# Kernel optimization log

Measured on AMD Instinct MI355X. Metric: run time of the kernel, lower is better.

The kernel has to match this reference:

```python
import jax, jax.numpy as jnp
import numpy as np

BATCH = 32768
DIM = 256
NUM_LATENTS = 4096
ENTROPY_WEIGHT = 0.1
VQ_BETA = 0.25
EPS = 1e-9


def _l2_normalize(v, axis=-1, eps=1e-12):
    # matches torch F.normalize(dim=-1)
    n = jnp.linalg.norm(v, axis=axis, keepdims=True)
    return v / jnp.maximum(n, eps)


def setup_inputs() -> dict:
    key = jax.random.key(0)
    kx, kc = jax.random.split(key)
    x = jax.random.normal(kx, (BATCH, DIM), dtype=jnp.float32)
    # codebook initialized uniform(-bound, bound) then row-normalized, as in __init__
    bound = (3.0 / DIM) ** 0.5
    cb = jax.random.uniform(kc, (NUM_LATENTS, DIM), dtype=jnp.float32,
                            minval=-bound, maxval=bound)
    codebook = _l2_normalize(cb)
    return {"x": x, "codebook": codebook}


def reference(x, codebook):
    # cosine-distance nearest-code lookup
    x_norm = _l2_normalize(x)                       # [B, D]
    cb_norm = _l2_normalize(codebook)               # [K, D]
    distance = -jnp.einsum('bd,kd->bk', x_norm, cb_norm)  # [B, K]
    # dropout p=0.0 -> identity
    indices = jnp.argmin(distance, axis=-1)         # [B] int
    z = codebook[indices]                           # [B, D] gather

    # straight-through estimator
    z_q = x + jax.lax.stop_gradient(z - x)

    commit_loss = jnp.mean((x - jax.lax.stop_gradient(z)) ** 2)
    q_loss = jnp.mean((z - jax.lax.stop_gradient(x)) ** 2)

    # entropy of codebook usage
    counts = jnp.bincount(indices, length=NUM_LATENTS).astype(jnp.float32)
    probs = counts / counts.sum()
    entropy = -jnp.sum(probs * jnp.log(jnp.clip(probs, EPS)))
    entropy_loss = -entropy

    vq_loss = q_loss + VQ_BETA * commit_loss + ENTROPY_WEIGHT * entropy_loss
    return (z_q, vq_loss, q_loss, commit_loss, entropy_loss, entropy, indices)
```

## Files before the change

### kernel.cpp

```cpp
#include <hip/hip_runtime.h>
#include <math.h>

#define BATCH 32768
#define DIM   256
#define NLAT  4096

typedef _Float16 f16x8 __attribute__((ext_vector_type(8)));
typedef float    f32x16 __attribute__((ext_vector_type(16)));

#define WS_CBH    0u
#define WS_CBINV  2097152u
#define WS_KEYS   2113536u
#define WS_HIST   4210688u

__device__ inline float kdec(uint key) {
  return __uint_as_float(key & 0xFFFFF000u);
}

__device__ inline void gload_lds16(const void* g, void* l) {
  __builtin_amdgcn_global_load_lds(
      (const __attribute__((address_space(1))) void*)g,
      (__attribute__((address_space(3))) void*)l, 16, 0, 0);
}

__global__ __launch_bounds__(256) void prep_kernel(
    const float* __restrict__ x, const float* __restrict__ cb,
    float* __restrict__ cbinv, uint4* __restrict__ cbhf4,
    uint4* __restrict__ xhf4, int* __restrict__ hist) {
  __shared__ __align__(16) uint4 lds[2048];
  __shared__ float linv[64];
  int bid = blockIdx.x, tid = threadIdx.x;
  if (bid < 64) {
    int w = tid >> 6, l = tid & 63;
    int t = bid;
    for (int rr = 0; rr < 16; ++rr) {
      int row = t * 64 + w * 16 + rr;
      float4 v = ((const float4*)(cb + (size_t)row * DIM))[l];
      float s = v.x * v.x + v.y * v.y + v.z * v.z + v.w * v.w;
      #pragma unroll
      for (int m = 32; m; m >>= 1) s += __shfl_xor(s, m, 64);
      if (l == 0) {
        float inv = 1.0f / fmaxf(sqrtf(s), 1e-12f);
        linv[w * 16 + rr] = inv;
        cbinv[row] = inv;
      }
    }
    __syncthreads();
    #pragma unroll
    for (int k = 0; k < 8; ++k) {
      int g = tid * 8 + k;
      int r64 = g >> 5, c = g & 31;
      const float4* cr = (const float4*)(cb + (size_t)(t * 64 + r64) * DIM);
      float inv = linv[r64];
      float4 a = cr[c * 2], b = cr[c * 2 + 1];
      union { _Float16 h[8]; uint4 u; } pk;
      pk.h[0] = (_Float16)(a.x * inv); pk.h[1] = (_Float16)(a.y * inv);
      pk.h[2] = (_Float16)(a.z * inv); pk.h[3] = (_Float16)(a.w * inv);
      pk.h[4] = (_Float16)(b.x * inv); pk.h[5] = (_Float16)(b.y * inv);
      pk.h[6] = (_Float16)(b.z * inv); pk.h[7] = (_Float16)(b.w * inv);
      int rf = r64 >> 5, row31 = r64 & 31;
      int sl = c >> 1, lhh = c & 1;
      lds[(sl * 2 + rf) * 64 + lhh * 32 + row31] = pk.u;
    }
    __syncthreads();
    uint4* outp = cbhf4 + (size_t)t * 2048;
    #pragma unroll
    for (int k = 0; k < 8; ++k)
      outp[tid * 8 + k] = lds[tid * 8 + k];
  } else if (bid < 1088) {
    int xb = bid - 64;
    const float4* xs = (const float4*)x + (size_t)xb * 2048;
    #pragma unroll
    for (int k = 0; k < 4; ++k) {
      int g = tid * 4 + k;
      float4 a = xs[g * 2];
      float4 b = xs[g * 2 + 1];
      union { _Float16 h[8]; uint4 u; } pk;
      pk.h[0] = (_Float16)a.x; pk.h[1] = (_Float16)a.y;
      pk.h[2] = (_Float16)a.z; pk.h[3] = (_Float16)a.w;
      pk.h[4] = (_Float16)b.x; pk.h[5] = (_Float16)b.y;
      pk.h[6] = (_Float16)b.z; pk.h[7] = (_Float16)b.w;
      int row31 = g >> 5, c = g & 31;
      lds[(c >> 1) * 64 + (c & 1) * 32 + row31] = pk.u;
    }
    __syncthreads();
    uint4* outp = xhf4 + (size_t)xb * 1024;
    #pragma unroll
    for (int k = 0; k < 4; ++k)
      outp[tid * 4 + k] = lds[tid * 4 + k];
  } else {
    for (int k = tid; k < NLAT; k += 256) hist[k] = 0;
  }
}

__global__ __launch_bounds__(256, 2) void vq_gemm_kernel(
    const char* __restrict__ xhf, const char* __restrict__ cbhf,
    uint* __restrict__ keys) {
  __shared__ __align__(16) char smem[65536];

  const int tid = threadIdx.x;
  const int w = tid >> 6, l = tid & 63;
  const int l31 = l & 31, lh = l >> 5;
  const int bb = blockIdx.x >> 2, q = blockIdx.x & 3;
  const int wrow0 = bb * 128 + w * 32;
  const int cbase = q * 1024;
  const uint lh4u = (uint)(lh << 2);

  const char* xb = xhf + ((size_t)(bb * 4 + w) * 1024 + (size_t)l) * 16;
  f16x8 xf[16];
  #pragma unroll
  for (int s2 = 0; s2 < 16; ++s2) xf[s2] = *(const f16x8*)(xb + s2 * 1024);

  const char* qbase = cbhf + (size_t)q * 524288;
  auto STAGE = [&](int bufoff, int t) {
    const char* src = qbase + t * 32768 + (size_t)tid * 16;
    char* dst = smem + bufoff + w * 1024;
    #pragma unroll
    for (int s = 0; s < 8; ++s)
      gload_lds16(src + s * 4096, dst + s * 4096);
  };

  STAGE(0, 0);
  asm volatile("s_waitcnt vmcnt(0)" ::: "memory");
  __syncthreads();

  uint k1 = 0, k2 = 0, k3 = 0;
  int curoff = 0;

  #pragma unroll 1
  for (int t = 0; t < 16; ++t) {
    if (t < 15) STAGE(curoff ^ 32768, t + 1);

    f32x16 acc[2];
    #pragma unroll
    for (int r = 0; r < 16; ++r) { acc[0][r] = 32.0f; acc[1][r] = 32.0f; }

    const char* bp = smem + curoff + (size_t)l * 16;
    #pragma unroll
    for (int sl = 0; sl < 16; ++sl) {
      f16x8 a0 = *(const f16x8*)(bp + (sl * 2) * 1024);
      f16x8 a1 = *(const f16x8*)(bp + (sl * 2 + 1) * 1024);
      acc[0] = __builtin_amdgcn_mfma_f32_32x32x16_f16(
          a0, xf[sl], acc[0], 0, 0, 0);
      acc[1] = __builtin_amdgcn_mfma_f32_32x32x16_f16(
          a1, xf[sl], acc[1], 0, 0, 0);
    }

    const uint scode = (uint)(cbase + t * 64);
    #pragma unroll
    for (int rf = 0; rf < 2; ++rf) {
      #pragma unroll
      for (int r = 0; r < 16; ++r) {
        const uint cr = (uint)(rf * 32 + (r & 3) + 8 * (r >> 2));
        uint key = (__float_as_uint(acc[rf][r]) & 0xFFFFF000u)
                 | scode | cr | lh4u;
        uint m1 = max(k1, key), n1 = min(k1, key); k1 = m1;
        uint m2 = max(k2, n1),  n2 = min(k2, n1);  k2 = m2;
        k3 = max(k3, n2);
      }
    }

    asm volatile("s_waitcnt vmcnt(0)" ::: "memory");
    __syncthreads();
    curoff ^= 32768;
  }

  uint o1 = __shfl_xor(k1, 32, 64);
  uint o2 = __shfl_xor(k2, 32, 64);
  uint o3 = __shfl_xor(k3, 32, 64);
  uint k4 = 0;
  #pragma unroll
  for (int e = 0; e < 3; ++e) {
    uint o = (e == 0) ? o1 : (e == 1) ? o2 : o3;
    uint m = max(k1, o), n = min(k1, o); k1 = m;
    m = max(k2, n); n = min(k2, n); k2 = m;
    m = max(k3, n); n = min(k3, n); k3 = m;
    k4 = max(k4, n);
  }
  if (lh == 0) {
    uint4 kv; kv.x = k1; kv.y = k2; kv.z = k3; kv.w = k4;
    *(uint4*)(keys + (size_t)(wrow0 + l31) * 16 + q * 4) = kv;
  }
}

__global__ __launch_bounds__(256) void rescore_kernel(
    const float* __restrict__ x, const float* __restrict__ cb,
    const float* __restrict__ cbinv, const uint* __restrict__ keys,
    float* __restrict__ zq, float* __restrict__ out_idx,
    int* __restrict__ hist, double* __restrict__ psse) {
  __shared__ float part[4];
  int tid = threadIdx.x, w = tid >> 6, l = tid & 63;
  int row = blockIdx.x * 4 + w;
  const float4* xr = (const float4*)(x + (size_t)row * DIM);
  float4 xv = xr[l];
  float s0 = xv.x * xv.x + xv.y * xv.y + xv.z * xv.z + xv.w * xv.w;
  #pragma unroll
  for (int m = 32; m; m >>= 1) s0 += __shfl_xor(s0, m, 64);
  float xnorm = sqrtf(s0);
  float xinv = 1.0f / fmaxf(xnorm, 1e-12f);

  uint key = keys[row * 16 + (l & 15)];
  uint kmax = key;
  #pragma unroll
  for (int m = 1; m < 16; m <<= 1) {
    uint o = __shfl_xor(kmax, m, 64);
    kmax = (o > kmax) ? o : kmax;
  }
  float dmax = kdec(kmax);
  float thr = dmax - 2.0f * (3e-3f * xnorm);
  bool inwin = (kdec(key) >= thr) && (l < 16);
  unsigned long long mask = __ballot(inwin);
  int besti;
  if (__popcll(mask) == 1) {
    besti = (int)(kmax & 0xFFFu);
  } else {
    float bestv = -3e38f; besti = 0x7fffffff;
    unsigned long long mm = mask;
    while (mm) {
      int b = __ffsll(mm) - 1; mm &= mm - 1;
      int ci = (int)(__shfl(key, b, 64) & 0xFFFu);
      float cbi = cbinv[ci];
      const float4* cr = (const float4*)(cb + (size_t)ci * DIM);
      float4 cv = cr[l];
      float d = (xv.x * xinv) * (cv.x * cbi) + (xv.y * xinv) * (cv.y * cbi)
              + (xv.z * xinv) * (cv.z * cbi) + (xv.w * xinv) * (cv.w * cbi);
      #pragma unroll
      for (int m = 32; m; m >>= 1) d += __shfl_xor(d, m, 64);
      bool better = (d > bestv) || (d == bestv && ci < besti);
      bestv = better ? d : bestv;
      besti = better ? ci : besti;
    }
  }

  float4 zv = ((const float4*)(cb + (size_t)besti * DIM))[l];
  float4 o;
  o.x = xv.x + (zv.x - xv.x); o.y = xv.y + (zv.y - xv.y);
  o.z = xv.z + (zv.z - xv.z); o.w = xv.w + (zv.w - xv.w);
  ((float4*)(zq + (size_t)row * DIM))[l] = o;
  float dx = xv.x - zv.x, dy = xv.y - zv.y, dz = xv.z - zv.z, dw = xv.w - zv.w;
  float s = dx * dx + dy * dy + dz * dz + dw * dw;
  #pragma unroll
  for (int m = 32; m; m >>= 1) s += __shfl_xor(s, m, 64);
  if (l == 0) part[w] = s;
  __syncthreads();
  if (tid == 0)
    psse[blockIdx.x] = (double)((part[0] + part[1]) + (part[2] + part[3]));
  if (l == 0) {
    atomicAdd(&hist[besti], 1);
    out_idx[row] = (float)besti;
  }
}

__global__ __launch_bounds__(256) void finalize_kernel(
    const int* __restrict__ hist, const double* __restrict__ psse,
    float* __restrict__ outs) {
  int tid = threadIdx.x;
  double e = 0.0, s = 0.0;
  for (int k = tid; k < NLAT; k += 256) {
    int c = hist[k];
    if (c > 0) {
      float p = (float)c * (1.0f / 32768.0f);
      e += (double)(p * logf(p));
    }
  }
  for (int k = tid; k < BATCH / 4; k += 256) s += psse[k];
  #pragma unroll
  for (int off = 32; off; off >>= 1) {
    e += __shfl_xor(e, off, 64);
    s += __shfl_xor(s, off, 64);
  }
  __shared__ double pe[4], ps[4];
  int w = tid >> 6, l = tid & 63;
  if (l == 0) { pe[w] = e; ps[w] = s; }
  __syncthreads();
  if (tid == 0) {
    double H = -((pe[0] + pe[1]) + (pe[2] + pe[3]));
    double sse = (ps[0] + ps[1]) + (ps[2] + ps[3]);
    double qv = sse * (1.0 / ((double)BATCH * (double)DIM));
    float qf = (float)qv;
    float Hf = (float)H;
    float ent_loss = -Hf;
    float vq = qf + 0.25f * qf + 0.1f * ent_loss;
    outs[0] = vq;
    outs[1] = qf;
    outs[2] = qf;
    outs[3] = ent_loss;
    outs[4] = Hf;
  }
}

extern "C" void kernel_launch(void* const* d_in, const int* in_sizes, int n_in,
                              void* d_out, int out_size, void* d_ws, size_t ws_size,
                              hipStream_t stream) {
  const float* x  = (const float*)d_in[0];
  const float* cb = (const float*)d_in[1];

  float* out     = (float*)d_out;
  float* zq      = out;
  float* scalars = out + (size_t)BATCH * DIM;
  float* oidx    = scalars + 5;

  char* wsb = (char*)d_ws;
  ushort* cbhf  = (ushort*)(wsb + WS_CBH);
  float*  cbinv = (float*)(wsb + WS_CBINV);
  uint*   keys  = (uint*)(wsb + WS_KEYS);
  int*    hist  = (int*)(wsb + WS_HIST);
  double* psse  = (double*)(wsb + WS_CBH);

  ushort* xhf = (ushort*)d_out;

  prep_kernel<<<1089, 256, 0, stream>>>(x, cb, cbinv, (uint4*)cbhf,
                                        (uint4*)xhf, hist);
  vq_gemm_kernel<<<1024, 256, 0, stream>>>((const char*)xhf,
                                           (const char*)cbhf, keys);
  rescore_kernel<<<BATCH / 4, 256, 0, stream>>>(x, cb, cbinv, keys,
                                                zq, oidx, hist, psse);
  finalize_kernel<<<1, 256, 0, stream>>>(hist, psse, scalars);
}
```

Before: 202.1 us.

## Fuse x fp16 conversion into GEMM kernel and reorder block-to-tile mapping

Drops the prep stage that converted x to fp16 into a swizzled workspace buffer. The GEMM kernel now reads fp32 rows of x directly and converts them to fp16 in registers, saving one full write and read of the converted x plus most of the prep grid. The block index mapping also changes so that consecutive blocks share a codebook quarter rather than an x tile, which changes L2 reuse of the codebook. The trade-off is that each GEMM block reads twice the bytes of x in fp32, through a less coalesced per-row access pattern.

After: 205.6 us. No clear change (+1.7%).

```diff
diff --git a/kernel.cpp b/kernel.cpp
--- a/kernel.cpp
+++ b/kernel.cpp
@@ -24,9 +24,8 @@
 }
 
 __global__ __launch_bounds__(256) void prep_kernel(
-    const float* __restrict__ x, const float* __restrict__ cb,
-    float* __restrict__ cbinv, uint4* __restrict__ cbhf4,
-    uint4* __restrict__ xhf4, int* __restrict__ hist) {
+    const float* __restrict__ cb, float* __restrict__ cbinv,
+    uint4* __restrict__ cbhf4, int* __restrict__ hist) {
   __shared__ __align__(16) uint4 lds[2048];
   __shared__ float linv[64];
   int bid = blockIdx.x, tid = threadIdx.x;
@@ -67,49 +66,36 @@
     #pragma unroll
     for (int k = 0; k < 8; ++k)
       outp[tid * 8 + k] = lds[tid * 8 + k];
-  } else if (bid < 1088) {
-    int xb = bid - 64;
-    const float4* xs = (const float4*)x + (size_t)xb * 2048;
-    #pragma unroll
-    for (int k = 0; k < 4; ++k) {
-      int g = tid * 4 + k;
-      float4 a = xs[g * 2];
-      float4 b = xs[g * 2 + 1];
-      union { _Float16 h[8]; uint4 u; } pk;
-      pk.h[0] = (_Float16)a.x; pk.h[1] = (_Float16)a.y;
-      pk.h[2] = (_Float16)a.z; pk.h[3] = (_Float16)a.w;
-      pk.h[4] = (_Float16)b.x; pk.h[5] = (_Float16)b.y;
-      pk.h[6] = (_Float16)b.z; pk.h[7] = (_Float16)b.w;
-      int row31 = g >> 5, c = g & 31;
-      lds[(c >> 1) * 64 + (c & 1) * 32 + row31] = pk.u;
-    }
-    __syncthreads();
-    uint4* outp = xhf4 + (size_t)xb * 1024;
-    #pragma unroll
-    for (int k = 0; k < 4; ++k)
-      outp[tid * 4 + k] = lds[tid * 4 + k];
   } else {
     for (int k = tid; k < NLAT; k += 256) hist[k] = 0;
   }
 }
 
 __global__ __launch_bounds__(256, 2) void vq_gemm_kernel(
-    const char* __restrict__ xhf, const char* __restrict__ cbhf,
+    const float* __restrict__ x, const char* __restrict__ cbhf,
     uint* __restrict__ keys) {
   __shared__ __align__(16) char smem[65536];
 
   const int tid = threadIdx.x;
   const int w = tid >> 6, l = tid & 63;
   const int l31 = l & 31, lh = l >> 5;
-  const int bb = blockIdx.x >> 2, q = blockIdx.x & 3;
+  const int bb = blockIdx.x & 255, q = blockIdx.x >> 8;
   const int wrow0 = bb * 128 + w * 32;
   const int cbase = q * 1024;
   const uint lh4u = (uint)(lh << 2);
 
-  const char* xb = xhf + ((size_t)(bb * 4 + w) * 1024 + (size_t)l) * 16;
+  const float4* xrow = (const float4*)(x + (size_t)(wrow0 + l31) * DIM)
+                     + lh * 2;
   f16x8 xf[16];
   #pragma unroll
-  for (int s2 = 0; s2 < 16; ++s2) xf[s2] = *(const f16x8*)(xb + s2 * 1024);
+  for (int s2 = 0; s2 < 16; ++s2) {
+    float4 a = xrow[s2 * 4];
+    float4 b = xrow[s2 * 4 + 1];
+    xf[s2][0] = (_Float16)a.x; xf[s2][1] = (_Float16)a.y;
+    xf[s2][2] = (_Float16)a.z; xf[s2][3] = (_Float16)a.w;
+    xf[s2][4] = (_Float16)b.x; xf[s2][5] = (_Float16)b.y;
+    xf[s2][6] = (_Float16)b.z; xf[s2][7] = (_Float16)b.w;
+  }
 
   const char* qbase = cbhf + (size_t)q * 524288;
   auto STAGE = [&](int bufoff, int t) {
@@ -307,12 +293,8 @@
   int*    hist  = (int*)(wsb + WS_HIST);
   double* psse  = (double*)(wsb + WS_CBH);
 
-  ushort* xhf = (ushort*)d_out;
-
-  prep_kernel<<<1089, 256, 0, stream>>>(x, cb, cbinv, (uint4*)cbhf,
-                                        (uint4*)xhf, hist);
-  vq_gemm_kernel<<<1024, 256, 0, stream>>>((const char*)xhf,
-                                           (const char*)cbhf, keys);
+  prep_kernel<<<65, 256, 0, stream>>>(cb, cbinv, (uint4*)cbhf, hist);
+  vq_gemm_kernel<<<1024, 256, 0, stream>>>(x, (const char*)cbhf, keys);
   rescore_kernel<<<BATCH / 4, 256, 0, stream>>>(x, cb, cbinv, keys,
                                                 zq, oidx, hist, psse);
   finalize_kernel<<<1, 256, 0, stream>>>(hist, psse, scalars);
```
